# Performance work log

Hardware: AMD Instinct MI355X
Metric: run time of the kernel (lower is better)

Reference implementation:

```python
import jax, jax.numpy as jnp
import numpy as np

HID = 128   # Config.hidden_dim
K = 16      # kNN neighbors in TempEdgeConv
BIG = 1e9


def _glu(x, wl, bl, wg, bg):
    return (x @ wl + bl) * jax.nn.sigmoid(x @ wg + bg)


def _temp_edge_conv(h, t, w, b, k):
    # h: [G,n,d] node features, t: [G,n,1] temporal key feature
    # dynamic kNN graph on temporal distance within each graph
    d = jnp.abs(t - jnp.swapaxes(t, 1, 2))                  # [G,n,n]
    n = h.shape[1]
    d = d + jnp.eye(n, dtype=h.dtype) * BIG                  # exclude self
    _, idx = jax.lax.top_k(-d, k)                            # [G,n,k]
    hj = jax.vmap(lambda hg, ig: hg[ig])(h, idx)             # [G,n,k,d] gather
    hi = jnp.broadcast_to(h[:, :, None, :], hj.shape)
    e = jnp.concatenate([hi, hj - hi], axis=-1)              # [G,n,k,2d]
    e = e @ w + b                                            # edge MLP
    return jnp.max(e, axis=2)                                # max aggregation


def setup_inputs():
    key = jax.random.key(0)
    ks = jax.random.split(key, 18)
    G, n, IN, H = 64, 1024, 17, HID
    N = G * n
    feat = IN - 1                  # 16
    temb = H // 4                  # 32

    def lin(k1, i, o):
        ka, kb = jax.random.split(k1)
        return (jax.random.normal(ka, (i, o), jnp.float32) / np.sqrt(i),
                jax.random.normal(kb, (o,), jnp.float32) * 0.01)

    x = jax.random.normal(ks[0], (N, IN), jnp.float32)
    batch = jnp.repeat(jnp.arange(G, dtype=jnp.int32), n)
    te_w, te_b = lin(ks[1], 1, temb)
    ig_lw, ig_lb = lin(ks[2], feat + temb, H)
    ig_gw, ig_gb = lin(ks[3], feat + temb, H)
    c1_w, c1_b = lin(ks[4], 2 * H, H)
    c2_w, c2_b = lin(ks[5], 2 * H, H)
    fg_lw, fg_lb = lin(ks[6], 4 * H, H)
    fg_gw, fg_gb = lin(ks[7], 4 * H, H)
    out_w, out_b = lin(ks[8], H, 2)
    return {"x": x, "te_w": te_w, "te_b": te_b,
            "ig_lw": ig_lw, "ig_lb": ig_lb, "ig_gw": ig_gw, "ig_gb": ig_gb,
            "c1_w": c1_w, "c1_b": c1_b, "c2_w": c2_w, "c2_b": c2_b,
            "fg_lw": fg_lw, "fg_lb": fg_lb, "fg_gw": fg_gw, "fg_gb": fg_gb,
            "out_w": out_w, "out_b": out_b,
            "batch": batch, "num_graphs": 64}


def reference(x, te_w, te_b, ig_lw, ig_lb, ig_gw, ig_gb,
              c1_w, c1_b, c2_w, c2_b, fg_lw, fg_lb, fg_gw, fg_gb,
              out_w, out_b, batch, num_graphs):
    G = int(num_graphs)
    N = x.shape[0]
    n = N // G   # equal-sized graphs (batch = repeat(arange(G), n))
    key_feat = x[:, :1]                       # key_feature_idx == 0
    feats = x[:, 1:]
    t_emb = key_feat @ te_w + te_b            # time encoder [N, H//4]
    h = _glu(jnp.concatenate([feats, t_emb], axis=-1),
             ig_lw, ig_lb, ig_gw, ig_gb)      # [N, H] (dropout = identity, eval)
    h = h.reshape(G, n, HID)
    t = key_feat.reshape(G, n, 1)
    x1 = jax.nn.relu(_temp_edge_conv(h, t, c1_w, c1_b, K))   # [G,n,H]
    x2 = jax.nn.relu(_temp_edge_conv(x1, t, c2_w, c2_b, K))  # [G,n,H]
    comb = jnp.concatenate([x1, x2], axis=-1)                # [G,n,2H]
    pooled = jnp.concatenate([comb.max(axis=1), comb.mean(axis=1)], axis=-1)  # [G,4H]
    logits = _glu(pooled, fg_lw, fg_lb, fg_gw, fg_gb) @ out_w + out_b
    return jax.nn.log_softmax(logits, axis=-1)
```

## Files before the change

kernel.cpp:

```cpp
#include <hip/hip_runtime.h>
#include <math.h>

#define NN 65536
#define NG 64
#define NPG 1024
#define HID 128
#define KNN 16
#define BINF 1e30f

typedef unsigned long long ull;
typedef _Float16 f16;
typedef _Float16 f16x8 __attribute__((ext_vector_type(8)));
typedef float f32x4 __attribute__((ext_vector_type(4)));

__global__ __launch_bounds__(1024) void k_topk(
    const float* __restrict__ x, int* __restrict__ sidxg,
    signed char* __restrict__ nbroff,
    const float* __restrict__ ig_lw, const float* __restrict__ ig_gw,
    const float* __restrict__ c1_w, const float* __restrict__ c2_w,
    f16* __restrict__ gfrag, f16* __restrict__ f1, f16* __restrict__ f2) {
    __shared__ ull key[1024];
    __shared__ float st[1024];
    __shared__ int sidx[1024];
    int g = blockIdx.x;
    if (g >= NG) {
        int gid = (g - NG) * 1024 + threadIdx.x;
        if (gid < 16384) {
            int i = gid & 7, lane = (gid >> 3) & 63, nt = (gid >> 9) & 7;
            int kt = (gid >> 12) & 1, mat = gid >> 13;
            int k = kt * 32 + ((lane >> 4) << 3) + i;
            int c = nt * 16 + (lane & 15);
            float v = 0.0f;
            if (k < 48) v = (mat ? ig_gw : ig_lw)[k * 128 + c];
            gfrag[gid] = (f16)v;
        } else {
            int g2 = gid - 16384;
            int buf = g2 >> 15;
            int rem = g2 & 32767;
            int mat = rem >> 14;
            int r2 = rem & 16383;
            int i = r2 & 7, lane = (r2 >> 3) & 63, nt = (r2 >> 9) & 7, kt = (r2 >> 12) & 3;
            int k = kt * 32 + ((lane >> 4) << 3) + i;
            int c = nt * 16 + (lane & 15);
            const float* cw = buf ? c2_w : c1_w;
            float top = cw[k * 128 + c];
            float bot = cw[(128 + k) * 128 + c];
            float v = mat ? bot : (top - bot);
            (buf ? f2 : f1)[rem] = (f16)v;
        }
        return;
    }
    int i = threadIdx.x;
    float t = x[(size_t)(g * NPG + i) * 17];
    unsigned ub = __float_as_uint(t);
    ub = (ub & 0x80000000u) ? ~ub : (ub | 0x80000000u);
    ull kk = ((ull)ub << 32) | (unsigned)i;

    for (int k = 2; k <= 1024; k <<= 1) {
        for (int j = k >> 1; j > 0; j >>= 1) {
            ull pv;
            if (j >= 64) {
                key[i] = kk;
                __syncthreads();
                pv = key[i ^ j];
                __syncthreads();
            } else {
                pv = __shfl_xor(kk, j, 64);
            }
            bool up = ((i & k) == 0);
            bool low = ((i & j) == 0);
            ull mn = kk < pv ? kk : pv;
            ull mx = kk < pv ? pv : kk;
            kk = (up == low) ? mn : mx;
        }
    }
    int oi = (int)(kk & 0xffffffffu);
    st[i] = x[(size_t)(g * NPG + oi) * 17];
    sidx[i] = oi;
    sidxg[g * NPG + i] = g * NPG + oi;
    __syncthreads();

    float tt = st[i];
    int L = i - 1, R = i + 1;
    signed char* out = nbroff + (size_t)(g * NPG + i) * KNN;
#pragma unroll
    for (int q = 0; q < KNN; q++) {
        float dl = (L >= 0)   ? (tt - st[L]) : BINF;
        float dr = (R < NPG) ? (st[R] - tt) : BINF;
        bool left;
        if (dl < dr) left = true;
        else if (dr < dl) left = false;
        else left = (sidx[L] < sidx[R]);
        int jr;
        if (left) { jr = L; L--; }
        else      { jr = R; R++; }
        out[q] = (signed char)(jr - i);
    }
}

__global__ __launch_bounds__(256) void k_fuse1(
    const float* __restrict__ x, const float* __restrict__ te_w,
    const float* __restrict__ te_b, const f16x8* __restrict__ gfrag,
    const float* __restrict__ bl, const float* __restrict__ bg,
    const int* __restrict__ sidxg, const f16x8* __restrict__ wfrag,
    const float* __restrict__ cb, f16* __restrict__ A, f16* __restrict__ B) {
    __shared__ f16x8 XL[4 * 2 * 64];
    __shared__ f16 ht[64 * 128];
    int tid = threadIdx.x;
    int r0 = blockIdx.x * 64;
#pragma unroll
    for (int p = 0; p < 2; p++) {
        int idx = tid + p * 256;
        int row = idx >> 3, kq = idx & 7;
        int node = sidxg[r0 + row];
        f16x8 h;
        if (kq < 2) {
            const float* xr = x + (size_t)node * 17 + 1 + kq * 8;
#pragma unroll
            for (int i = 0; i < 8; i++) h[i] = (f16)xr[i];
        } else if (kq < 6) {
            float t = x[(size_t)node * 17];
            int j0 = (kq - 2) * 8;
#pragma unroll
            for (int i = 0; i < 8; i++) h[i] = (f16)fmaf(t, te_w[j0 + i], te_b[j0 + i]);
        } else {
#pragma unroll
            for (int i = 0; i < 8; i++) h[i] = (f16)0.0f;
        }
        int mf = row >> 4, kt = kq >> 2, lane = ((kq & 3) << 4) | (row & 15);
        XL[(mf * 2 + kt) * 64 + lane] = h;
    }
    __syncthreads();
    int w = tid >> 6, lane = tid & 63;
    f32x4 acc[2][2][4];
#pragma unroll
    for (int o = 0; o < 2; o++)
#pragma unroll
        for (int j = 0; j < 2; j++)
#pragma unroll
            for (int mf = 0; mf < 4; mf++) acc[o][j][mf] = (f32x4){0.f, 0.f, 0.f, 0.f};
#pragma unroll 1
    for (int kt = 0; kt < 2; kt++) {
        f16x8 wf0[2], wf1[2], xa[4];
#pragma unroll
        for (int j = 0; j < 2; j++) {
            wf0[j] = gfrag[((0 * 2 + kt) * 8 + (w * 2 + j)) * 64 + lane];
            wf1[j] = gfrag[((1 * 2 + kt) * 8 + (w * 2 + j)) * 64 + lane];
        }
#pragma unroll
        for (int mf = 0; mf < 4; mf++) xa[mf] = XL[(mf * 2 + kt) * 64 + lane];
#pragma unroll
        for (int mf = 0; mf < 4; mf++)
#pragma unroll
            for (int j = 0; j < 2; j++) {
                acc[0][j][mf] = __builtin_amdgcn_mfma_f32_16x16x32_f16(xa[mf], wf0[j], acc[0][j][mf], 0, 0, 0);
                acc[1][j][mf] = __builtin_amdgcn_mfma_f32_16x16x32_f16(xa[mf], wf1[j], acc[1][j][mf], 0, 0, 0);
            }
    }
#pragma unroll
    for (int j = 0; j < 2; j++) {
        int col = w * 32 + j * 16 + (lane & 15);
        float bbl = bl[col], bbg = bg[col];
#pragma unroll
        for (int mf = 0; mf < 4; mf++) {
            int rloc = mf * 16 + ((lane >> 4) << 2);
#pragma unroll
            for (int q = 0; q < 4; q++) {
                float lin = acc[0][j][mf][q] + bbl;
                float gat = acc[1][j][mf][q] + bbg;
                int row = rloc + q;
                ht[(row * 128 + col) ^ ((row & 7) << 3)] = (f16)(lin / (1.0f + expf(-gat)));
            }
        }
    }
    __syncthreads();
#pragma unroll
    for (int o = 0; o < 2; o++)
#pragma unroll
        for (int j = 0; j < 2; j++)
#pragma unroll
            for (int mf = 0; mf < 4; mf++) acc[o][j][mf] = (f32x4){0.f, 0.f, 0.f, 0.f};
    int row16 = lane & 15, kslot = lane >> 4;
    int swz = (row16 & 7) << 3;
#pragma unroll 1
    for (int kt = 0; kt < 4; kt++) {
        f16x8 wf0[2], wf1[2], xa[4];
#pragma unroll
        for (int j = 0; j < 2; j++) {
            wf0[j] = wfrag[((0 * 4 + kt) * 8 + (w * 2 + j)) * 64 + lane];
            wf1[j] = wfrag[((1 * 4 + kt) * 8 + (w * 2 + j)) * 64 + lane];
        }
#pragma unroll
        for (int mf = 0; mf < 4; mf++)
            xa[mf] = *(const f16x8*)&ht[((mf * 16 + row16) * 128 + kt * 32 + kslot * 8) ^ swz];
#pragma unroll
        for (int mf = 0; mf < 4; mf++)
#pragma unroll
            for (int j = 0; j < 2; j++) {
                acc[0][j][mf] = __builtin_amdgcn_mfma_f32_16x16x32_f16(xa[mf], wf0[j], acc[0][j][mf], 0, 0, 0);
                acc[1][j][mf] = __builtin_amdgcn_mfma_f32_16x16x32_f16(xa[mf], wf1[j], acc[1][j][mf], 0, 0, 0);
            }
    }
#pragma unroll
    for (int j = 0; j < 2; j++) {
        int col = w * 32 + j * 16 + (lane & 15);
        float bias = cb[col];
#pragma unroll
        for (int mf = 0; mf < 4; mf++) {
            int rbase = r0 + mf * 16 + ((lane >> 4) << 2);
#pragma unroll
            for (int q = 0; q < 4; q++) {
                A[(size_t)(rbase + q) * 128 + col] = (f16)(acc[0][j][mf][q] + bias);
                B[(size_t)(rbase + q) * 128 + col] = (f16)acc[1][j][mf][q];
            }
        }
    }
}

__global__ __launch_bounds__(256) void k_conv2f(
    const f16* __restrict__ A1, const f16* __restrict__ B1,
    const signed char* __restrict__ nbroff, const f16x8* __restrict__ wfrag,
    const float* __restrict__ cb, f16* __restrict__ A2, f16* __restrict__ B2,
    float* __restrict__ partM1, float* __restrict__ partS1) {
    __shared__ f16 Bwin[96 * 128];
    __shared__ f16 x1t[64 * 128];
    __shared__ float redM[4 * 128];
    __shared__ float redS[4 * 128];
    int tid = threadIdx.x;
    int bx = blockIdx.x;
    int r0 = bx * 64;
    int r0loc = (bx & 15) * 64;
#pragma unroll
    for (int p = 0; p < 6; p++) {
        int idx = tid + p * 256;
        int row = idx >> 4, kq = idx & 15;
        int gl = r0loc - 16 + row;
        f16x8 v;
#pragma unroll
        for (int i = 0; i < 8; i++) v[i] = (f16)0.0f;
        if (gl >= 0 && gl < NPG)
            v = *(const f16x8*)(B1 + (size_t)(r0 - 16 + row) * 128 + kq * 8);
        *(f16x8*)&Bwin[row * 128 + kq * 8] = v;
    }
    __syncthreads();
    int w = tid >> 6, lane = tid & 63;
    int rquad = lane >> 4;
    int c0 = (lane & 15) * 8;
    float pm[8], ps[8];
#pragma unroll
    for (int i = 0; i < 8; i++) { pm[i] = -BINF; ps[i] = 0.f; }
#pragma unroll 1
    for (int rr = 0; rr < 4; rr++) {
        int row = w * 16 + rr * 4 + rquad;
        int grow = r0 + row;
        int4 ov = *(const int4*)(nbroff + (size_t)grow * 16);
        const int* ow = (const int*)&ov;
        f16x8 m;
#pragma unroll
        for (int i = 0; i < 8; i++) m[i] = (f16)(-INFINITY);
        const char* bbase = (const char*)Bwin + (size_t)(row + 16) * 256 + c0 * 2;
#pragma unroll
        for (int q = 0; q < 16; q++) {
            int off = (int)(signed char)((ow[q >> 2] >> ((q & 3) * 8)) & 0xff);
            f16x8 bv = *(const f16x8*)(bbase + off * 256);
            m = __builtin_elementwise_max(m, bv);
        }
        f16x8 av = *(const f16x8*)(A1 + (size_t)grow * 128 + c0);
        f16x8 ou;
#pragma unroll
        for (int i = 0; i < 8; i++) {
            float v = fmaxf((float)av[i] + (float)m[i], 0.0f);
            pm[i] = fmaxf(pm[i], v);
            ps[i] += v;
            ou[i] = (f16)v;
        }
        int idx = (row * 128 + c0) ^ ((row & 7) << 3);
        *(f16x8*)&x1t[idx] = ou;
    }
#pragma unroll
    for (int i = 0; i < 8; i++) {
        pm[i] = fmaxf(pm[i], __shfl_xor(pm[i], 16));
        pm[i] = fmaxf(pm[i], __shfl_xor(pm[i], 32));
        ps[i] += __shfl_xor(ps[i], 16);
        ps[i] += __shfl_xor(ps[i], 32);
    }
    if (rquad == 0) {
#pragma unroll
        for (int i = 0; i < 8; i++) {
            redM[w * 128 + c0 + i] = pm[i];
            redS[w * 128 + c0 + i] = ps[i];
        }
    }
    __syncthreads();
    if (tid < 128) {
        float M = -BINF, S = 0.f;
#pragma unroll
        for (int w2 = 0; w2 < 4; w2++) {
            M = fmaxf(M, redM[w2 * 128 + tid]);
            S += redS[w2 * 128 + tid];
        }
        partM1[(size_t)bx * 128 + tid] = M;
        partS1[(size_t)bx * 128 + tid] = S;
    }
    f32x4 acc[2][2][4];
#pragma unroll
    for (int o = 0; o < 2; o++)
#pragma unroll
        for (int j = 0; j < 2; j++)
#pragma unroll
            for (int mf = 0; mf < 4; mf++) acc[o][j][mf] = (f32x4){0.f, 0.f, 0.f, 0.f};
    int row16 = lane & 15, kslot = lane >> 4;
    int swz = (row16 & 7) << 3;
#pragma unroll 1
    for (int kt = 0; kt < 4; kt++) {
        f16x8 wf0[2], wf1[2], xa[4];
#pragma unroll
        for (int j = 0; j < 2; j++) {
            wf0[j] = wfrag[((0 * 4 + kt) * 8 + (w * 2 + j)) * 64 + lane];
            wf1[j] = wfrag[((1 * 4 + kt) * 8 + (w * 2 + j)) * 64 + lane];
        }
#pragma unroll
        for (int mf = 0; mf < 4; mf++)
            xa[mf] = *(const f16x8*)&x1t[((mf * 16 + row16) * 128 + kt * 32 + kslot * 8) ^ swz];
#pragma unroll
        for (int mf = 0; mf < 4; mf++)
#pragma unroll
            for (int j = 0; j < 2; j++) {
                acc[0][j][mf] = __builtin_amdgcn_mfma_f32_16x16x32_f16(xa[mf], wf0[j], acc[0][j][mf], 0, 0, 0);
                acc[1][j][mf] = __builtin_amdgcn_mfma_f32_16x16x32_f16(xa[mf], wf1[j], acc[1][j][mf], 0, 0, 0);
            }
    }
#pragma unroll
    for (int j = 0; j < 2; j++) {
        int col = w * 32 + j * 16 + (lane & 15);
        float bias = cb[col];
#pragma unroll
        for (int mf = 0; mf < 4; mf++) {
            int rbase = r0 + mf * 16 + ((lane >> 4) << 2);
#pragma unroll
            for (int q = 0; q < 4; q++) {
                A2[(size_t)(rbase + q) * 128 + col] = (f16)(acc[0][j][mf][q] + bias);
                B2[(size_t)(rbase + q) * 128 + col] = (f16)acc[1][j][mf][q];
            }
        }
    }
}

__global__ __launch_bounds__(256) void k_gather2p(
    const f16* __restrict__ A2, const f16* __restrict__ B2,
    const signed char* __restrict__ nbroff,
    float* __restrict__ partM2, float* __restrict__ partS2) {
    __shared__ f16 Bwin[96 * 128];
    __shared__ float redM[4 * 128];
    __shared__ float redS[4 * 128];
    int tid = threadIdx.x;
    int bx = blockIdx.x;
    int r0 = bx * 64;
    int r0loc = (bx & 15) * 64;
#pragma unroll
    for (int p = 0; p < 6; p++) {
        int idx = tid + p * 256;
        int row = idx >> 4, kq = idx & 15;
        int gl = r0loc - 16 + row;
        f16x8 v;
#pragma unroll
        for (int i = 0; i < 8; i++) v[i] = (f16)0.0f;
        if (gl >= 0 && gl < NPG)
            v = *(const f16x8*)(B2 + (size_t)(r0 - 16 + row) * 128 + kq * 8);
        *(f16x8*)&Bwin[row * 128 + kq * 8] = v;
    }
    __syncthreads();
    int w = tid >> 6, lane = tid & 63;
    int rquad = lane >> 4;
    int c0 = (lane & 15) * 8;
    float pm[8], ps[8];
#pragma unroll
    for (int i = 0; i < 8; i++) { pm[i] = -BINF; ps[i] = 0.f; }
#pragma unroll 1
    for (int rr = 0; rr < 4; rr++) {
        int row = w * 16 + rr * 4 + rquad;
        int grow = r0 + row;
        int4 ov = *(const int4*)(nbroff + (size_t)grow * 16);
        const int* ow = (const int*)&ov;
        f16x8 m;
#pragma unroll
        for (int i = 0; i < 8; i++) m[i] = (f16)(-INFINITY);
        const char* bbase = (const char*)Bwin + (size_t)(row + 16) * 256 + c0 * 2;
#pragma unroll
        for (int q = 0; q < 16; q++) {
            int off = (int)(signed char)((ow[q >> 2] >> ((q & 3) * 8)) & 0xff);
            f16x8 bv = *(const f16x8*)(bbase + off * 256);
            m = __builtin_elementwise_max(m, bv);
        }
        f16x8 av = *(const f16x8*)(A2 + (size_t)grow * 128 + c0);
#pragma unroll
        for (int i = 0; i < 8; i++) {
            float v = fmaxf((float)av[i] + (float)m[i], 0.0f);
            pm[i] = fmaxf(pm[i], v);
            ps[i] += v;
        }
    }
#pragma unroll
    for (int i = 0; i < 8; i++) {
        pm[i] = fmaxf(pm[i], __shfl_xor(pm[i], 16));
        pm[i] = fmaxf(pm[i], __shfl_xor(pm[i], 32));
        ps[i] += __shfl_xor(ps[i], 16);
        ps[i] += __shfl_xor(ps[i], 32);
    }
    if (rquad == 0) {
#pragma unroll
        for (int i = 0; i < 8; i++) {
            redM[w * 128 + c0 + i] = pm[i];
            redS[w * 128 + c0 + i] = ps[i];
        }
    }
    __syncthreads();
    if (tid < 128) {
        float M = -BINF, S = 0.f;
#pragma unroll
        for (int w2 = 0; w2 < 4; w2++) {
            M = fmaxf(M, redM[w2 * 128 + tid]);
            S += redS[w2 * 128 + tid];
        }
        partM2[(size_t)bx * 128 + tid] = M;
        partS2[(size_t)bx * 128 + tid] = S;
    }
}

__global__ __launch_bounds__(256) void k_final(const float* __restrict__ partM1,
                                               const float* __restrict__ partS1,
                                               const float* __restrict__ partM2,
                                               const float* __restrict__ partS2,
                                               const float* __restrict__ fg_lw,
                                               const float* __restrict__ fg_lb,
                                               const float* __restrict__ fg_gw,
                                               const float* __restrict__ fg_gb,
                                               const float* __restrict__ out_w,
                                               const float* __restrict__ out_b,
                                               float* __restrict__ out) {
    __shared__ float pooled[512];
    __shared__ float linv[128], gatev[128];
    __shared__ float gluv[128];
    __shared__ float lg[2];
    int g = blockIdx.x, tid = threadIdx.x;

    const float* pM = (tid < 128) ? partM1 : partM2;
    const float* pS = (tid < 128) ? partS1 : partS2;
    int cc = tid & 127;
    float mx = -BINF, sm = 0.0f;
    for (int ch = 0; ch < 16; ch++) {
        mx = fmaxf(mx, pM[(size_t)(g * 16 + ch) * 128 + cc]);
        sm += pS[(size_t)(g * 16 + ch) * 128 + cc];
    }
    pooled[tid] = mx;
    pooled[256 + tid] = sm * (1.0f / 1024.0f);
    __syncthreads();

    float acc = 0.0f;
    if (tid < 128) {
        for (int k = 0; k < 512; k++) acc = fmaf(pooled[k], fg_lw[k * 128 + tid], acc);
        linv[tid] = acc + fg_lb[tid];
    } else {
        int c = tid - 128;
        for (int k = 0; k < 512; k++) acc = fmaf(pooled[k], fg_gw[k * 128 + c], acc);
        gatev[c] = acc + fg_gb[c];
    }
    __syncthreads();
    if (tid < 128) gluv[tid] = linv[tid] / (1.0f + expf(-gatev[tid]));
    __syncthreads();
    if (tid < 2) {
        float s = out_b[tid];
        for (int c = 0; c < 128; c++) s = fmaf(gluv[c], out_w[c * 2 + tid], s);
        lg[tid] = s;
    }
    __syncthreads();
    if (tid < 2) {
        float m = fmaxf(lg[0], lg[1]);
        float lse = m + logf(expf(lg[0] - m) + expf(lg[1] - m));
        out[g * 2 + tid] = lg[tid] - lse;
    }
}

extern "C" void kernel_launch(void* const* d_in, const int* in_sizes, int n_in,
                              void* d_out, int out_size, void* d_ws, size_t ws_size,
                              hipStream_t stream) {
    const float* x     = (const float*)d_in[0];
    const float* te_w  = (const float*)d_in[1];
    const float* te_b  = (const float*)d_in[2];
    const float* ig_lw = (const float*)d_in[3];
    const float* ig_lb = (const float*)d_in[4];
    const float* ig_gw = (const float*)d_in[5];
    const float* ig_gb = (const float*)d_in[6];
    const float* c1_w  = (const float*)d_in[7];
    const float* c1_b  = (const float*)d_in[8];
    const float* c2_w  = (const float*)d_in[9];
    const float* c2_b  = (const float*)d_in[10];
    const float* fg_lw = (const float*)d_in[11];
    const float* fg_lb = (const float*)d_in[12];
    const float* fg_gw = (const float*)d_in[13];
    const float* fg_gb = (const float*)d_in[14];
    const float* out_w = (const float*)d_in[15];
    const float* out_b = (const float*)d_in[16];
    float* out = (float*)d_out;

    char* p = (char*)d_ws;
    const size_t T16 = (size_t)NN * HID * sizeof(f16);
    f16* A1 = (f16*)p; p += T16;
    f16* B1 = (f16*)p; p += T16;
    f16* A2 = (f16*)p; p += T16;
    f16* B2 = (f16*)p; p += T16;
    int* sidxg = (int*)p;            p += (size_t)NN * 4;
    signed char* nbroff = (signed char*)p; p += (size_t)NN * KNN;
    float* partM1 = (float*)p;       p += (size_t)1024 * 128 * 4;
    float* partS1 = (float*)p;       p += (size_t)1024 * 128 * 4;
    float* partM2 = (float*)p;       p += (size_t)1024 * 128 * 4;
    float* partS2 = (float*)p;       p += (size_t)1024 * 128 * 4;
    f16* gfrag = (f16*)p;            p += 16384 * 2;
    f16* f1 = (f16*)p;               p += 32768 * 2;
    f16* f2 = (f16*)p;               p += 32768 * 2;

    k_topk<<<NG + 80, 1024, 0, stream>>>(x, sidxg, nbroff, ig_lw, ig_gw,
                                         c1_w, c2_w, gfrag, f1, f2);
    k_fuse1<<<NN / 64, 256, 0, stream>>>(x, te_w, te_b, (const f16x8*)gfrag,
                                         ig_lb, ig_gb, sidxg, (const f16x8*)f1,
                                         c1_b, A1, B1);
    k_conv2f<<<NN / 64, 256, 0, stream>>>(A1, B1, nbroff, (const f16x8*)f2,
                                          c2_b, A2, B2, partM1, partS1);
    k_gather2p<<<NN / 64, 256, 0, stream>>>(A2, B2, nbroff, partM2, partS2);
    k_final<<<NG, 256, 0, stream>>>(partM1, partS1, partM2, partS2,
                                    fg_lw, fg_lb, fg_gw, fg_gb, out_w, out_b, out);
}
```

Baseline: 105.2 us.

## Fuse conv2 edge-MLP and second gather into one kernel with halo recompute

Merges k_conv2f and k_gather2p into a single kernel that keeps layer-2 A/B activations in LDS instead of writing them to global memory and reading them back. Each block recomputes x1 and the conv2 projection for a 16-row halo on each side (96 rows instead of 64), so neighbor lookups for the second gather stay block-local. The LDS row stride is padded to 272 bytes to cut bank conflicts. The trade is 50% extra gather and MFMA work per block, about 79KB of LDS per block that limits occupancy, and more accumulator registers, in exchange for removing one launch and the A2/B2 global round trip.

```diff
diff --git a/kernel.cpp b/kernel.cpp
--- a/kernel.cpp
+++ b/kernel.cpp
@@ -7,6 +7,7 @@
 #define HID 128
 #define KNN 16
 #define BINF 1e30f
+#define BWS 272
 
 typedef unsigned long long ull;
 typedef _Float16 f16;
@@ -217,62 +218,76 @@
     }
 }
 
-__global__ __launch_bounds__(256) void k_conv2f(
+__global__ __launch_bounds__(256) void k_megac2(
     const f16* __restrict__ A1, const f16* __restrict__ B1,
     const signed char* __restrict__ nbroff, const f16x8* __restrict__ wfrag,
-    const float* __restrict__ cb, f16* __restrict__ A2, f16* __restrict__ B2,
-    float* __restrict__ partM1, float* __restrict__ partS1) {
-    __shared__ f16 Bwin[96 * 128];
-    __shared__ f16 x1t[64 * 128];
-    __shared__ float redM[4 * 128];
-    __shared__ float redS[4 * 128];
+    const float* __restrict__ cb,
+    float* __restrict__ partM1, float* __restrict__ partS1,
+    float* __restrict__ partM2, float* __restrict__ partS2) {
+    __shared__ char SM[80896];
+    char* bw  = SM;
+    char* b2  = SM;
+    f16*  x1t = (f16*)(SM + 34816);
+    char* a2  = SM + 59392;
+    float* redM = (float*)(SM + 76800);
+    float* redS = (float*)(SM + 78848);
+
     int tid = threadIdx.x;
     int bx = blockIdx.x;
     int r0 = bx * 64;
     int r0loc = (bx & 15) * 64;
-#pragma unroll
-    for (int p = 0; p < 6; p++) {
+    int gbase = r0 - r0loc;
+
+#pragma unroll
+    for (int p = 0; p < 8; p++) {
         int idx = tid + p * 256;
         int row = idx >> 4, kq = idx & 15;
-        int gl = r0loc - 16 + row;
+        int gl = r0loc - 32 + row;
         f16x8 v;
 #pragma unroll
         for (int i = 0; i < 8; i++) v[i] = (f16)0.0f;
         if (gl >= 0 && gl < NPG)
-            v = *(const f16x8*)(B1 + (size_t)(r0 - 16 + row) * 128 + kq * 8);
-        *(f16x8*)&Bwin[row * 128 + kq * 8] = v;
-    }
-    __syncthreads();
+            v = *(const f16x8*)(B1 + (size_t)(gbase + gl) * 128 + kq * 8);
+        *(f16x8*)(bw + row * BWS + kq * 16) = v;
+    }
+    __syncthreads();
+
     int w = tid >> 6, lane = tid & 63;
     int rquad = lane >> 4;
     int c0 = (lane & 15) * 8;
+
     float pm[8], ps[8];
 #pragma unroll
     for (int i = 0; i < 8; i++) { pm[i] = -BINF; ps[i] = 0.f; }
 #pragma unroll 1
-    for (int rr = 0; rr < 4; rr++) {
-        int row = w * 16 + rr * 4 + rquad;
-        int grow = r0 + row;
-        int4 ov = *(const int4*)(nbroff + (size_t)grow * 16);
-        const int* ow = (const int*)&ov;
-        f16x8 m;
-#pragma unroll
-        for (int i = 0; i < 8; i++) m[i] = (f16)(-INFINITY);
-        const char* bbase = (const char*)Bwin + (size_t)(row + 16) * 256 + c0 * 2;
-#pragma unroll
-        for (int q = 0; q < 16; q++) {
-            int off = (int)(signed char)((ow[q >> 2] >> ((q & 3) * 8)) & 0xff);
-            f16x8 bv = *(const f16x8*)(bbase + off * 256);
-            m = __builtin_elementwise_max(m, bv);
-        }
-        f16x8 av = *(const f16x8*)(A1 + (size_t)grow * 128 + c0);
+    for (int rr = 0; rr < 6; rr++) {
+        int row = w * 24 + rr * 4 + rquad;
+        int gl = r0loc - 16 + row;
         f16x8 ou;
 #pragma unroll
-        for (int i = 0; i < 8; i++) {
-            float v = fmaxf((float)av[i] + (float)m[i], 0.0f);
-            pm[i] = fmaxf(pm[i], v);
-            ps[i] += v;
-            ou[i] = (f16)v;
+        for (int i = 0; i < 8; i++) ou[i] = (f16)0.0f;
+        if (gl >= 0 && gl < NPG) {
+            int grow = gbase + gl;
+            int4 ov = *(const int4*)(nbroff + (size_t)grow * 16);
+            const int* ow = (const int*)&ov;
+            f16x8 m;
+#pragma unroll
+            for (int i = 0; i < 8; i++) m[i] = (f16)(-INFINITY);
+#pragma unroll
+            for (int q = 0; q < 16; q++) {
+                int off = (int)(signed char)((ow[q >> 2] >> ((q & 3) * 8)) & 0xff);
+                int hn = row + 16 + off;
+                f16x8 bv = *(const f16x8*)(bw + hn * BWS + c0 * 2);
+                m = __builtin_elementwise_max(m, bv);
+            }
+            f16x8 av = *(const f16x8*)(A1 + (size_t)grow * 128 + c0);
+            bool interior = (row >= 16) && (row < 80);
+#pragma unroll
+            for (int i = 0; i < 8; i++) {
+                float v = fmaxf((float)av[i] + (float)m[i], 0.0f);
+                ou[i] = (f16)v;
+                if (interior) { pm[i] = fmaxf(pm[i], v); ps[i] += v; }
+            }
         }
         int idx = (row * 128 + c0) ^ ((row & 7) << 3);
         *(f16x8*)&x1t[idx] = ou;
@@ -302,28 +317,29 @@
         partM1[(size_t)bx * 128 + tid] = M;
         partS1[(size_t)bx * 128 + tid] = S;
     }
-    f32x4 acc[2][2][4];
+
+    f32x4 acc[2][2][6];
 #pragma unroll
     for (int o = 0; o < 2; o++)
 #pragma unroll
         for (int j = 0; j < 2; j++)
 #pragma unroll
-            for (int mf = 0; mf < 4; mf++) acc[o][j][mf] = (f32x4){0.f, 0.f, 0.f, 0.f};
+            for (int mf = 0; mf < 6; mf++) acc[o][j][mf] = (f32x4){0.f, 0.f, 0.f, 0.f};
     int row16 = lane & 15, kslot = lane >> 4;
     int swz = (row16 & 7) << 3;
 #pragma unroll 1
     for (int kt = 0; kt < 4; kt++) {
-        f16x8 wf0[2], wf1[2], xa[4];
+        f16x8 wf0[2], wf1[2], xa[6];
 #pragma unroll
         for (int j = 0; j < 2; j++) {
             wf0[j] = wfrag[((0 * 4 + kt) * 8 + (w * 2 + j)) * 64 + lane];
             wf1[j] = wfrag[((1 * 4 + kt) * 8 + (w * 2 + j)) * 64 + lane];
         }
 #pragma unroll
-        for (int mf = 0; mf < 4; mf++)
+        for (int mf = 0; mf < 6; mf++)
             xa[mf] = *(const f16x8*)&x1t[((mf * 16 + row16) * 128 + kt * 32 + kslot * 8) ^ swz];
 #pragma unroll
-        for (int mf = 0; mf < 4; mf++)
+        for (int mf = 0; mf < 6; mf++)
 #pragma unroll
             for (int j = 0; j < 2; j++) {
                 acc[0][j][mf] = __builtin_amdgcn_mfma_f32_16x16x32_f16(xa[mf], wf0[j], acc[0][j][mf], 0, 0, 0);
@@ -335,64 +351,38 @@
         int col = w * 32 + j * 16 + (lane & 15);
         float bias = cb[col];
 #pragma unroll
-        for (int mf = 0; mf < 4; mf++) {
-            int rbase = r0 + mf * 16 + ((lane >> 4) << 2);
+        for (int mf = 0; mf < 6; mf++) {
+            int rloc = mf * 16 + ((lane >> 4) << 2);
 #pragma unroll
             for (int q = 0; q < 4; q++) {
-                A2[(size_t)(rbase + q) * 128 + col] = (f16)(acc[0][j][mf][q] + bias);
-                B2[(size_t)(rbase + q) * 128 + col] = (f16)acc[1][j][mf][q];
-            }
-        }
-    }
-}
-
-__global__ __launch_bounds__(256) void k_gather2p(
-    const f16* __restrict__ A2, const f16* __restrict__ B2,
-    const signed char* __restrict__ nbroff,
-    float* __restrict__ partM2, float* __restrict__ partS2) {
-    __shared__ f16 Bwin[96 * 128];
-    __shared__ float redM[4 * 128];
-    __shared__ float redS[4 * 128];
-    int tid = threadIdx.x;
-    int bx = blockIdx.x;
-    int r0 = bx * 64;
-    int r0loc = (bx & 15) * 64;
-#pragma unroll
-    for (int p = 0; p < 6; p++) {
-        int idx = tid + p * 256;
-        int row = idx >> 4, kq = idx & 15;
-        int gl = r0loc - 16 + row;
-        f16x8 v;
-#pragma unroll
-        for (int i = 0; i < 8; i++) v[i] = (f16)0.0f;
-        if (gl >= 0 && gl < NPG)
-            v = *(const f16x8*)(B2 + (size_t)(r0 - 16 + row) * 128 + kq * 8);
-        *(f16x8*)&Bwin[row * 128 + kq * 8] = v;
-    }
-    __syncthreads();
-    int w = tid >> 6, lane = tid & 63;
-    int rquad = lane >> 4;
-    int c0 = (lane & 15) * 8;
-    float pm[8], ps[8];
+                int hrow = rloc + q;
+                *(f16*)(b2 + hrow * BWS + col * 2) = (f16)acc[1][j][mf][q];
+                if (hrow >= 16 && hrow < 80)
+                    *(f16*)(a2 + (hrow - 16) * BWS + col * 2) = (f16)(acc[0][j][mf][q] + bias);
+            }
+        }
+    }
+    __syncthreads();
+
 #pragma unroll
     for (int i = 0; i < 8; i++) { pm[i] = -BINF; ps[i] = 0.f; }
 #pragma unroll 1
     for (int rr = 0; rr < 4; rr++) {
-        int row = w * 16 + rr * 4 + rquad;
-        int grow = r0 + row;
+        int rl = w * 16 + rr * 4 + rquad;
+        int grow = r0 + rl;
         int4 ov = *(const int4*)(nbroff + (size_t)grow * 16);
         const int* ow = (const int*)&ov;
         f16x8 m;
 #pragma unroll
         for (int i = 0; i < 8; i++) m[i] = (f16)(-INFINITY);
-        const char* bbase = (const char*)Bwin + (size_t)(row + 16) * 256 + c0 * 2;
 #pragma unroll
         for (int q = 0; q < 16; q++) {
             int off = (int)(signed char)((ow[q >> 2] >> ((q & 3) * 8)) & 0xff);
-            f16x8 bv = *(const f16x8*)(bbase + off * 256);
+            int hn = rl + 16 + off;
+            f16x8 bv = *(const f16x8*)(b2 + hn * BWS + c0 * 2);
             m = __builtin_elementwise_max(m, bv);
         }
-        f16x8 av = *(const f16x8*)(A2 + (size_t)grow * 128 + c0);
+        f16x8 av = *(const f16x8*)(a2 + rl * BWS + c0 * 2);
 #pragma unroll
         for (int i = 0; i < 8; i++) {
             float v = fmaxf((float)av[i] + (float)m[i], 0.0f);
@@ -407,6 +397,7 @@
         ps[i] += __shfl_xor(ps[i], 16);
         ps[i] += __shfl_xor(ps[i], 32);
     }
+    __syncthreads();
     if (rquad == 0) {
 #pragma unroll
         for (int i = 0; i < 8; i++) {
@@ -507,8 +498,6 @@
     const size_t T16 = (size_t)NN * HID * sizeof(f16);
     f16* A1 = (f16*)p; p += T16;
     f16* B1 = (f16*)p; p += T16;
-    f16* A2 = (f16*)p; p += T16;
-    f16* B2 = (f16*)p; p += T16;
     int* sidxg = (int*)p;            p += (size_t)NN * 4;
     signed char* nbroff = (signed char*)p; p += (size_t)NN * KNN;
     float* partM1 = (float*)p;       p += (size_t)1024 * 128 * 4;
@@ -524,9 +513,8 @@
     k_fuse1<<<NN / 64, 256, 0, stream>>>(x, te_w, te_b, (const f16x8*)gfrag,
                                          ig_lb, ig_gb, sidxg, (const f16x8*)f1,
                                          c1_b, A1, B1);
-    k_conv2f<<<NN / 64, 256, 0, stream>>>(A1, B1, nbroff, (const f16x8*)f2,
-                                          c2_b, A2, B2, partM1, partS1);
-    k_gather2p<<<NN / 64, 256, 0, stream>>>(A2, B2, nbroff, partM2, partS2);
+    k_megac2<<<NN / 64, 256, 0, stream>>>(A1, B1, nbroff, (const f16x8*)f2,
+                                          c2_b, partM1, partS1, partM2, partS2);
     k_final<<<NG, 256, 0, stream>>>(partM1, partS1, partM2, partS2,
                                     fg_lw, fg_lb, fg_gw, fg_gb, out_w, out_b, out);
 }
```

Result: no change. 107.1 us (+1.8%).
